# Performance work log

Measured on AMD Instinct MI355X. Metric: run time of the kernel, lower is better.

Reference implementation:

```python
import jax, jax.numpy as jnp
import numpy as np

RADIUS = 0.2
K = 32       # nsample
S = 1024     # npoint
BN_EPS = 1e-5


def fps(xyz, s):
    # xyz: [B, N, 3] -> indices [B, s] (farthest point sampling, start at index 0)
    B, N, _ = xyz.shape

    def step(carry, _):
        dist, last = carry                                  # [B,N], [B]
        lp = jnp.take_along_axis(xyz, last[:, None, None], axis=1)  # [B,1,3]
        d = jnp.sum((xyz - lp) ** 2, axis=-1)               # [B,N]
        dist = jnp.minimum(dist, d)
        nxt = jnp.argmax(dist, axis=-1).astype(jnp.int32)
        return (dist, nxt), last

    init = (jnp.full((B, N), jnp.inf, xyz.dtype), jnp.zeros((B,), jnp.int32))
    _, idxs = jax.lax.scan(step, init, None, length=s)      # [s, B]
    return idxs.T                                           # [B, s]


def query_ball(new_xyz, xyz, radius, k):
    # new_xyz: [B,S,3], xyz: [B,N,3] -> first k in-ball indices [B,S,k]
    B, N, _ = xyz.shape
    d2 = jnp.sum((new_xyz[:, :, None, :] - xyz[:, None, :, :]) ** 2, axis=-1)  # [B,S,N]
    cand = jnp.where(d2 <= radius * radius, jnp.arange(N, dtype=jnp.int32)[None, None, :], N)
    idx = jnp.sort(cand, axis=-1)[..., :k]                  # first-k by index, pytorch3d order
    first = idx[..., :1]
    idx = jnp.where(idx == N, first, idx)                   # replicate first valid index
    return jnp.minimum(idx, N - 1)


def gather_pts(pts, idx):
    # pts: [B,N,C], idx: [B,S,K] -> [B,S,K,C]
    B, N, C = pts.shape
    _, s, k = idx.shape
    g = jnp.take_along_axis(pts, idx.reshape(B, s * k, 1), axis=1)
    return g.reshape(B, s, k, C)


def conv_bn_relu(x, W, b, g, be):
    # x: [B,S,K,Cin], W: [Cout,Cin] (1x1 conv), training-mode BatchNorm over (B,S,K)
    y = jnp.einsum('bskc,oc->bsko', x, W) + b
    mu = jnp.mean(y, axis=(0, 1, 2))
    var = jnp.var(y, axis=(0, 1, 2))
    y = (y - mu) * jax.lax.rsqrt(var + BN_EPS) * g + be
    return jax.nn.relu(y)


def setup_inputs() -> dict:
    key = jax.random.key(0)
    ks = jax.random.split(key, 8)
    B, N, D = 8, 8192, 64
    inp = {
        'xyz': jax.random.uniform(ks[0], (B, 3, N), dtype=jnp.float32),
        'points': jax.random.normal(ks[1], (B, D, N), dtype=jnp.float32),
    }
    dims = [(64, 67), (64, 64), (128, 64)]
    for i, (o, c) in enumerate(dims):
        inp[f'W{i}'] = jax.random.normal(ks[2 + i], (o, c), dtype=jnp.float32) * 0.05
        inp[f'b{i}'] = jnp.zeros((o,), jnp.float32)
        inp[f'g{i}'] = jnp.ones((o,), jnp.float32)
        inp[f'be{i}'] = jnp.zeros((o,), jnp.float32)
    return inp


def reference(xyz, points, W0, b0, g0, be0, W1, b1, g1, be1, W2, b2, g2, be2):
    # xyz: [B,3,N], points: [B,D,N]
    xyz_n = jnp.transpose(xyz, (0, 2, 1))                   # [B,N,3]
    pts_n = jnp.transpose(points, (0, 2, 1))                # [B,N,D]
    idx = fps(xyz_n, S)                                     # [B,S]
    new_xyz = jnp.take_along_axis(xyz_n, idx[..., None], axis=1)  # [B,S,3]
    gidx = query_ball(new_xyz, xyz_n, RADIUS, K)            # [B,S,K]
    gxyz = (gather_pts(xyz_n, gidx) - new_xyz[:, :, None, :]) / RADIUS  # [B,S,K,3]
    gpts = gather_pts(pts_n, gidx)                          # [B,S,K,D]
    feat = jnp.concatenate([gpts, gxyz], axis=-1)           # [B,S,K,D+3]
    feat = conv_bn_relu(feat, W0, b0, g0, be0)
    feat = conv_bn_relu(feat, W1, b1, g1, be1)
    feat = conv_bn_relu(feat, W2, b2, g2, be2)
    new_points = jnp.max(feat, axis=2)                      # [B,S,Cout]
    return (jnp.transpose(new_xyz, (0, 2, 1)), jnp.transpose(new_points, (0, 2, 1)))
```

## Files before the change

### kernel.cpp

```cpp
#include <hip/hip_runtime.h>

#define BB 8
#define NN 8192
#define SS 1024
#define KK 32
#define NPIX (BB*SS*KK)
#define R2C 0.04f
#define EPS 1e-5f

#define FT 1024
#define FW (FT/64)
#define PPT (NN/FT)
#define NCELL 4096
#define TBLK 64

#define OFF_IDX      0u
#define OFF_NEWXYZ   (OFF_IDX + BB*SS*4)
#define OFF_GIDX     (OFF_NEWXYZ + BB*SS*3*4)
#define OFF_XYZN     (OFF_GIDX + BB*SS*KK*4)
#define OFF_PTSN     (OFF_XYZN + BB*NN*3*4)
#define OFF_Y0       (OFF_PTSN + BB*NN*64*4)
#define OFF_Y1       (OFF_Y0 + NPIX*64*2)
#define OFF_MAXMIN   (OFF_Y1 + NPIX*64*2)
#define OFF_P0       (OFF_MAXMIN + BB*SS*128*2*4)
#define OFF_P1       (OFF_P0 + 1024*128*4)
#define OFF_P2       (OFF_P1 + 1024*128*4)
#define OFF_SC       (OFF_P2 + 1024*256*4)

__device__ __forceinline__ unsigned short f2bf(float x){
    unsigned u = __float_as_uint(x);
    unsigned r = (u + 0x7FFFu + ((u >> 16) & 1u)) >> 16;
    return (unsigned short)r;
}
__device__ __forceinline__ float bf2f(unsigned h){
    return __uint_as_float(h << 16);
}
__device__ __forceinline__ float sqdist3(float dx, float dy, float dz){
    return __fadd_rn(__fadd_rn(__fmul_rn(dx,dx), __fmul_rn(dy,dy)), __fmul_rn(dz,dz));
}
__device__ __forceinline__ int spread4(int v){
    return (v&1) | ((v&2)<<2) | ((v&4)<<4) | ((v&8)<<6);
}

template<int CTRL>
__device__ __forceinline__ unsigned long long dpp_max_step(unsigned long long k){
    int lo = (int)(unsigned)k;
    int hi = (int)(unsigned)(k >> 32);
    int olo = __builtin_amdgcn_update_dpp(0, lo, CTRL, 0xf, 0xf, true);
    int ohi = __builtin_amdgcn_update_dpp(0, hi, CTRL, 0xf, 0xf, true);
    unsigned long long o = ((unsigned long long)(unsigned)ohi << 32) | (unsigned)olo;
    return (o > k) ? o : k;
}
__device__ __forceinline__ unsigned long long wave_max_u64(unsigned long long k){
    k = dpp_max_step<0x111>(k);
    k = dpp_max_step<0x112>(k);
    k = dpp_max_step<0x114>(k);
    k = dpp_max_step<0x118>(k);
    k = dpp_max_step<0x142>(k);
    k = dpp_max_step<0x143>(k);
    return k;
}

__global__ __launch_bounds__(FT) void fps_kernel(const float* __restrict__ xyz,
                                                 const float* __restrict__ pts,
                                                 float* __restrict__ newxyz,
                                                 float* __restrict__ out,
                                                 float* __restrict__ xyz_n,
                                                 float* __restrict__ pts_n){
    __shared__ float sx[NN], sy[NN], sz[NN];
    __shared__ int   si[NN];
    __shared__ int   hist[NCELL];
    __shared__ int   waveTot[FW];
    __shared__ unsigned long long cells[SS];
    int tid = threadIdx.x;

    if (blockIdx.x >= 8){
        int gid = (blockIdx.x - 8) * FT + tid;
        int b = gid >> 13, i = gid & (NN - 1);
        const float* xb = xyz + (size_t)b * 3 * NN;
        float x = xb[i], y = xb[NN + i], z = xb[2 * NN + i];
        float* xd = xyz_n + ((size_t)b * NN + i) * 3;
        xd[0] = x; xd[1] = y; xd[2] = z;
        const float* pb = pts + (size_t)b * 64 * NN + i;
        float4* pd = (float4*)(pts_n + ((size_t)b * NN + i) * 64);
#pragma unroll
        for (int q = 0; q < 16; ++q){
            float4 v;
            v.x = pb[(q*4+0)*NN]; v.y = pb[(q*4+1)*NN];
            v.z = pb[(q*4+2)*NN]; v.w = pb[(q*4+3)*NN];
            pd[q] = v;
        }
        return;
    }

    int b = blockIdx.x;
    int wave = tid >> 6, lane = tid & 63;
    const float* xb = xyz + (size_t)b * 3 * NN;

    int cell[PPT];
#pragma unroll
    for (int j = 0; j < PPT; ++j){
        int i = tid + j * FT;
        float x = xb[i], y = xb[NN + i], z = xb[2*NN + i];
        sx[i] = x; sy[i] = y; sz[i] = z;
        int cx = min(15, max(0, (int)(x * 16.f)));
        int cy = min(15, max(0, (int)(y * 16.f)));
        int cz = min(15, max(0, (int)(z * 16.f)));
        cell[j] = spread4(cx) | (spread4(cy) << 1) | (spread4(cz) << 2);
    }
#pragma unroll
    for (int k = 0; k < NCELL/FT; ++k) hist[tid * (NCELL/FT) + k] = 0;
    cells[tid] = 0ull;
    __syncthreads();
#pragma unroll
    for (int j = 0; j < PPT; ++j) atomicAdd(&hist[cell[j]], 1);
    __syncthreads();
    {
        int base0 = tid * (NCELL/FT);
        int sum4 = 0;
#pragma unroll
        for (int k = 0; k < NCELL/FT; ++k) sum4 += hist[base0 + k];
        int s = sum4;
#pragma unroll
        for (int m = 1; m < 64; m <<= 1){
            int v = __shfl_up(s, m);
            if (lane >= m) s += v;
        }
        if (lane == 63) waveTot[wave] = s;
        __syncthreads();
        int wbase = 0;
#pragma unroll
        for (int w2 = 0; w2 < FW; ++w2) if (w2 < wave) wbase += waveTot[w2];
        int run = wbase + s - sum4;
#pragma unroll
        for (int k = 0; k < NCELL/FT; ++k){
            int h = hist[base0 + k];
            hist[base0 + k] = run;
            run += h;
        }
    }
    __syncthreads();
#pragma unroll
    for (int j = 0; j < PPT; ++j){
        int pos = atomicAdd(&hist[cell[j]], 1);
        si[pos] = tid + j * FT;
    }
    __syncthreads();
    float px[PPT], py[PPT], pz[PPT], dist[PPT];
    int oi[PPT];
    float bxmin =  1e30f, bxmax = -1e30f;
    float bymin =  1e30f, bymax = -1e30f;
    float bzmin =  1e30f, bzmax = -1e30f;
#pragma unroll
    for (int j = 0; j < PPT; ++j){
        int g = si[tid * PPT + j];
        oi[j] = g;
        float x = sx[g], y = sy[g], z = sz[g];
        px[j] = x; py[j] = y; pz[j] = z;
        bxmin = fminf(bxmin, x); bxmax = fmaxf(bxmax, x);
        bymin = fminf(bymin, y); bymax = fmaxf(bymax, y);
        bzmin = fminf(bzmin, z); bzmax = fmaxf(bzmax, z);
        dist[j] = __int_as_float(0x7f800000);
    }
    __syncthreads();

    unsigned long long mykey = 0ull;
    unsigned long long lane63cache = 0ull;
    float tmax = __int_as_float(0x7f800000);
    int w = 0;
    for (int t = 0; t < SS; ++t){
        if (tid == 0) hist[t] = w;
        float lx = sx[w], ly = sy[w], lz = sz[w];
        float cdx = __fsub_rn(lx, fminf(fmaxf(lx, bxmin), bxmax));
        float cdy = __fsub_rn(ly, fminf(fmaxf(ly, bymin), bymax));
        float cdz = __fsub_rn(lz, fminf(fmaxf(lz, bzmin), bzmax));
        float d_bb = sqdist3(cdx, cdy, cdz);
        bool active = d_bb < tmax;
        unsigned long long bal = __ballot(active);
        if (active){
            {
#pragma clang fp contract(off)
#pragma unroll
                for (int j = 0; j < PPT; ++j){
                    float dx = px[j] - lx;
                    float dy = py[j] - ly;
                    float dz = pz[j] - lz;
                    float d = ((dx*dx) + (dy*dy)) + (dz*dz);
                    dist[j] = fminf(dist[j], d);
                }
            }
            float m0 = fmaxf(dist[0], dist[1]);
            float m1 = fmaxf(dist[2], dist[3]);
            float m2 = fmaxf(dist[4], dist[5]);
            float m3 = fmaxf(dist[6], dist[7]);
            m0 = fmaxf(m0, m1); m2 = fmaxf(m2, m3);
            float maxd = fmaxf(m0, m2);
            int bo = 0x7fffffff;
#pragma unroll
            for (int j = 0; j < PPT; ++j)
                if (dist[j] == maxd) bo = min(bo, oi[j]);
            mykey = ((unsigned long long)__float_as_uint(maxd) << 32)
                  | (unsigned)(~bo);
            tmax = maxd;
        }
        if (bal){
            unsigned long long k = wave_max_u64(mykey);
            if (lane == 63) lane63cache = k;
        }
        if (lane == 63) atomicMax(&cells[t], lane63cache);
        __syncthreads();
        unsigned long long km = cells[t];
        w = (int)(~(unsigned)km);
    }
    __syncthreads();
    for (int t2 = tid; t2 < SS; t2 += FT){
        int hw = hist[t2];
        float x = sx[hw], y = sy[hw], z = sz[hw];
        out[(size_t)b * 3 * SS + t2]          = x;
        out[(size_t)b * 3 * SS + SS + t2]     = y;
        out[(size_t)b * 3 * SS + 2*SS + t2]   = z;
        float* nw = newxyz + ((size_t)b * SS + t2) * 3;
        nw[0] = x; nw[1] = y; nw[2] = z;
    }
}

__global__ __launch_bounds__(256) void qb_kernel(const float* __restrict__ xyz,
                                                 const float* __restrict__ newxyz,
                                                 int* __restrict__ gidx){
    int wid = (blockIdx.x * 256 + threadIdx.x) >> 6;
    int lane = threadIdx.x & 63;
    int b = wid >> 10;
    const float* nw = newxyz + (size_t)wid * 3;
    float cx = nw[0], cy = nw[1], cz = nw[2];
    const float* xb = xyz + (size_t)b * 3 * NN;
    int total = 0, firstIdx = -1;
    int* gout = gidx + (size_t)wid * KK;
    for (int base = 0; base < NN; base += 64){
        int i = base + lane;
        float dx = __fsub_rn(cx, xb[i]);
        float dy = __fsub_rn(cy, xb[NN + i]);
        float dz = __fsub_rn(cz, xb[2*NN + i]);
        float d2 = sqdist3(dx, dy, dz);
        bool in = (d2 <= R2C);
        unsigned long long m = __ballot(in);
        int pos = total + __popcll(m & ((1ull << lane) - 1ull));
        if (in && pos < KK) gout[pos] = i;
        if (firstIdx < 0 && m) firstIdx = base + (__ffsll((unsigned long long)m) - 1);
        total += __popcll(m);
        if (total >= KK) break;
    }
    if (total < KK){
        int f = (total > 0) ? firstIdx : (NN - 1);
        for (int p = total + lane; p < KK; p += 64) gout[p] = f;
    }
}

__global__ __launch_bounds__(256) void l0_kernel(const float* __restrict__ pts_n,
                                                 const float* __restrict__ xyz_n,
                                                 const float* __restrict__ newxyz,
                                                 const int* __restrict__ gidx,
                                                 const float* __restrict__ W0,
                                                 const float* __restrict__ b0,
                                                 uint4* __restrict__ y0,
                                                 float* __restrict__ part0){
    __shared__ float lsum[4][64][2];
    int tid = threadIdx.x;
    int pixel = blockIdx.x * 256 + tid;
    int sample = pixel >> 5;
    int b = sample >> 10;
    int gi = gidx[pixel];
    int wave = tid >> 6, lane = tid & 63;

    float ff[67];
    const float4* prow = (const float4*)(pts_n + ((size_t)b * NN + gi) * 64);
#pragma unroll
    for (int q = 0; q < 16; ++q){
        float4 v = prow[q];
        ff[q*4] = v.x; ff[q*4+1] = v.y; ff[q*4+2] = v.z; ff[q*4+3] = v.w;
    }
    const float* pr = xyz_n + ((size_t)b * NN + gi) * 3;
    const float* nw = newxyz + (size_t)sample * 3;
    ff[64] = __fsub_rn(pr[0], nw[0]) / 0.2f;
    ff[65] = __fsub_rn(pr[1], nw[1]) / 0.2f;
    ff[66] = __fsub_rn(pr[2], nw[2]) / 0.2f;

    for (int oc = 0; oc < 8; ++oc){
        float acc[8];
#pragma unroll
        for (int j = 0; j < 8; ++j) acc[j] = b0[oc*8+j];
#pragma unroll
        for (int c = 0; c < 67; ++c){
            float fe = ff[c];
#pragma unroll
            for (int j = 0; j < 8; ++j) acc[j] += fe * W0[(oc*8+j)*67 + c];
        }
        uint4 pk;
        unsigned us[8];
#pragma unroll
        for (int j = 0; j < 8; ++j){
            float v = acc[j];
            float s1 = v, s2 = v * v;
#pragma unroll
            for (int m = 1; m <= 32; m <<= 1){
                s1 += __shfl_xor(s1, m);
                s2 += __shfl_xor(s2, m);
            }
            if (lane == 0){ lsum[wave][oc*8+j][0] = s1; lsum[wave][oc*8+j][1] = s2; }
            us[j] = f2bf(v);
        }
        pk.x = us[0] | (us[1] << 16);
        pk.y = us[2] | (us[3] << 16);
        pk.z = us[4] | (us[5] << 16);
        pk.w = us[6] | (us[7] << 16);
        y0[(size_t)pixel * 8 + oc] = pk;
    }
    __syncthreads();
    if (tid < 128){
        float s = lsum[0][tid>>1][tid&1] + lsum[1][tid>>1][tid&1]
                + lsum[2][tid>>1][tid&1] + lsum[3][tid>>1][tid&1];
        part0[(size_t)blockIdx.x * 128 + tid] = s;
    }
}

__global__ __launch_bounds__(256) void l1_kernel(const uint4* __restrict__ y0,
                                                 const float* __restrict__ scale0,
                                                 const float* __restrict__ shift0,
                                                 const float* __restrict__ W1,
                                                 const float* __restrict__ b1,
                                                 uint4* __restrict__ y1,
                                                 float* __restrict__ part1){
    __shared__ float lsum[4][64][2];
    int tid = threadIdx.x;
    int pixel = blockIdx.x * 256 + tid;
    int wave = tid >> 6, lane = tid & 63;

    float x[64];
#pragma unroll
    for (int q = 0; q < 8; ++q){
        uint4 v = y0[(size_t)pixel * 8 + q];
        unsigned w[4] = {v.x, v.y, v.z, v.w};
#pragma unroll
        for (int r = 0; r < 4; ++r){
            int c = q*8 + r*2;
            x[c]   = fmaxf(bf2f(w[r] & 0xFFFFu) * scale0[c]   + shift0[c],   0.f);
            x[c+1] = fmaxf(bf2f(w[r] >> 16)     * scale0[c+1] + shift0[c+1], 0.f);
        }
    }
    for (int oc = 0; oc < 8; ++oc){
        float acc[8];
#pragma unroll
        for (int j = 0; j < 8; ++j) acc[j] = b1[oc*8+j];
#pragma unroll
        for (int c = 0; c < 64; ++c){
            float fe = x[c];
#pragma unroll
            for (int j = 0; j < 8; ++j) acc[j] += fe * W1[(oc*8+j)*64 + c];
        }
        uint4 pk;
        unsigned us[8];
#pragma unroll
        for (int j = 0; j < 8; ++j){
            float v = acc[j];
            float s1 = v, s2 = v * v;
#pragma unroll
            for (int m = 1; m <= 32; m <<= 1){
                s1 += __shfl_xor(s1, m);
                s2 += __shfl_xor(s2, m);
            }
            if (lane == 0){ lsum[wave][oc*8+j][0] = s1; lsum[wave][oc*8+j][1] = s2; }
            us[j] = f2bf(v);
        }
        pk.x = us[0] | (us[1] << 16);
        pk.y = us[2] | (us[3] << 16);
        pk.z = us[4] | (us[5] << 16);
        pk.w = us[6] | (us[7] << 16);
        y1[(size_t)pixel * 8 + oc] = pk;
    }
    __syncthreads();
    if (tid < 128){
        float s = lsum[0][tid>>1][tid&1] + lsum[1][tid>>1][tid&1]
                + lsum[2][tid>>1][tid&1] + lsum[3][tid>>1][tid&1];
        part1[(size_t)blockIdx.x * 128 + tid] = s;
    }
}

__global__ __launch_bounds__(256) void l2_kernel(const uint4* __restrict__ y1,
                                                 const float* __restrict__ scale1,
                                                 const float* __restrict__ shift1,
                                                 const float* __restrict__ W2,
                                                 const float* __restrict__ b2,
                                                 float* __restrict__ maxmin,
                                                 float* __restrict__ part2){
    __shared__ float lsum[4][128][2];
    int tid = threadIdx.x;
    int pixel = blockIdx.x * 256 + tid;
    int sample = pixel >> 5;
    int wave = tid >> 6, lane = tid & 63;

    float x[64];
#pragma unroll
    for (int q = 0; q < 8; ++q){
        uint4 v = y1[(size_t)pixel * 8 + q];
        unsigned w[4] = {v.x, v.y, v.z, v.w};
#pragma unroll
        for (int r = 0; r < 4; ++r){
            int c = q*8 + r*2;
            x[c]   = fmaxf(bf2f(w[r] & 0xFFFFu) * scale1[c]   + shift1[c],   0.f);
            x[c+1] = fmaxf(bf2f(w[r] >> 16)     * scale1[c+1] + shift1[c+1], 0.f);
        }
    }
    for (int oc = 0; oc < 16; ++oc){
        float acc[8];
#pragma unroll
        for (int j = 0; j < 8; ++j) acc[j] = b2[oc*8+j];
#pragma unroll
        for (int c = 0; c < 64; ++c){
            float fe = x[c];
#pragma unroll
            for (int j = 0; j < 8; ++j) acc[j] += fe * W2[(oc*8+j)*64 + c];
        }
#pragma unroll
        for (int j = 0; j < 8; ++j){
            float v = acc[j];
            int ch = oc*8 + j;
            float mx = v, mn = v;
#pragma unroll
            for (int m = 1; m <= 16; m <<= 1){
                mx = fmaxf(mx, __shfl_xor(mx, m));
                mn = fminf(mn, __shfl_xor(mn, m));
            }
            float s1 = v, s2 = v * v;
#pragma unroll
            for (int m = 1; m <= 32; m <<= 1){
                s1 += __shfl_xor(s1, m);
                s2 += __shfl_xor(s2, m);
            }
            if (lane == 0){ lsum[wave][ch][0] = s1; lsum[wave][ch][1] = s2; }
            if ((tid & 31) == 0){
                float* mm = maxmin + ((size_t)sample * 128 + ch) * 2;
                mm[0] = mx; mm[1] = mn;
            }
        }
    }
    __syncthreads();
    {
        float s = lsum[0][tid>>1][tid&1] + lsum[1][tid>>1][tid&1]
                + lsum[2][tid>>1][tid&1] + lsum[3][tid>>1][tid&1];
        part2[(size_t)blockIdx.x * 256 + tid] = s;
    }
}

__global__ __launch_bounds__(1024) void fin_kernel(const float* __restrict__ part, int O,
                           const float* __restrict__ g, const float* __restrict__ be,
                           float* __restrict__ scale, float* __restrict__ shift){
    __shared__ float4 ls[1024];
    int tid = threadIdx.x;
    int M = 2 * O;
    int V = M >> 2;
    int NC = 1024 / V;
    int q = tid & (V - 1);
    int c = tid / V;
    int per = 1024 / NC;
    const float4* p4 = (const float4*)part;
    float4 s = {0.f, 0.f, 0.f, 0.f};
    for (int r = 0; r < per; ++r){
        int blk = c * per + r;
        float4 v = p4[(size_t)blk * V + q];
        s.x += v.x; s.y += v.y; s.z += v.z; s.w += v.w;
    }
    ls[c * V + q] = s;
    __syncthreads();
    if (tid < V){
        float4 t4 = ls[tid];
        for (int c2 = 1; c2 < NC; ++c2){
            float4 v = ls[c2 * V + tid];
            t4.x += v.x; t4.y += v.y; t4.z += v.z; t4.w += v.w;
        }
        float inv = 1.0f / (float)NPIX;
        int ch0 = 2 * tid, ch1 = 2 * tid + 1;
        float mu0 = t4.x * inv;
        float var0 = t4.y * inv - mu0 * mu0;
        float sc0 = (1.0f / sqrtf(var0 + EPS)) * g[ch0];
        scale[ch0] = sc0; shift[ch0] = be[ch0] - mu0 * sc0;
        float mu1 = t4.z * inv;
        float var1 = t4.w * inv - mu1 * mu1;
        float sc1 = (1.0f / sqrtf(var1 + EPS)) * g[ch1];
        scale[ch1] = sc1; shift[ch1] = be[ch1] - mu1 * sc1;
    }
}

__global__ __launch_bounds__(256) void out_kernel(const float* __restrict__ maxmin,
                                                  const float* __restrict__ scale2,
                                                  const float* __restrict__ shift2,
                                                  float* __restrict__ out){
    int gid = blockIdx.x * 256 + threadIdx.x;
    int s = gid & 1023;
    int o = (gid >> 10) & 127;
    int b = gid >> 17;
    int sample = b * 1024 + s;
    float2 mm = ((const float2*)maxmin)[(size_t)sample * 128 + o];
    float sc = scale2[o], sh = shift2[o];
    float v = (sc >= 0.f) ? mm.x : mm.y;
    out[gid] = fmaxf(v * sc + sh, 0.f);
}

extern "C" void kernel_launch(void* const* d_in, const int* in_sizes, int n_in,
                              void* d_out, int out_size, void* d_ws, size_t ws_size,
                              hipStream_t stream) {
    const float* xyz = (const float*)d_in[0];
    const float* pts = (const float*)d_in[1];
    const float* W0 = (const float*)d_in[2];
    const float* b0 = (const float*)d_in[3];
    const float* g0 = (const float*)d_in[4];
    const float* be0 = (const float*)d_in[5];
    const float* W1 = (const float*)d_in[6];
    const float* b1 = (const float*)d_in[7];
    const float* g1 = (const float*)d_in[8];
    const float* be1 = (const float*)d_in[9];
    const float* W2 = (const float*)d_in[10];
    const float* b2 = (const float*)d_in[11];
    const float* g2 = (const float*)d_in[12];
    const float* be2 = (const float*)d_in[13];

    char* ws = (char*)d_ws;
    float* newxyz = (float*)(ws + OFF_NEWXYZ);
    int*   gidx   = (int*)(ws + OFF_GIDX);
    float* xyz_n  = (float*)(ws + OFF_XYZN);
    float* pts_n  = (float*)(ws + OFF_PTSN);
    uint4* y0     = (uint4*)(ws + OFF_Y0);
    uint4* y1     = (uint4*)(ws + OFF_Y1);
    float* maxmin = (float*)(ws + OFF_MAXMIN);
    float* part0  = (float*)(ws + OFF_P0);
    float* part1  = (float*)(ws + OFF_P1);
    float* part2  = (float*)(ws + OFF_P2);
    float* sc     = (float*)(ws + OFF_SC);
    float* scale0 = sc,        *shift0 = sc + 64;
    float* scale1 = sc + 128,  *shift1 = sc + 192;
    float* scale2 = sc + 256,  *shift2 = sc + 384;

    float* out = (float*)d_out;
    float* out_np = out + BB * 3 * SS;

    hipLaunchKernelGGL(fps_kernel, dim3(8 + TBLK), dim3(FT), 0, stream,
                       xyz, pts, newxyz, out, xyz_n, pts_n);
    hipLaunchKernelGGL(qb_kernel, dim3(2048), dim3(256), 0, stream, xyz, newxyz, gidx);
    hipLaunchKernelGGL(l0_kernel, dim3(1024), dim3(256), 0, stream,
                       pts_n, xyz_n, newxyz, gidx, W0, b0, y0, part0);
    hipLaunchKernelGGL(fin_kernel, dim3(1), dim3(1024), 0, stream, part0, 64, g0, be0, scale0, shift0);
    hipLaunchKernelGGL(l1_kernel, dim3(1024), dim3(256), 0, stream,
                       y0, scale0, shift0, W1, b1, y1, part1);
    hipLaunchKernelGGL(fin_kernel, dim3(1), dim3(1024), 0, stream, part1, 64, g1, be1, scale1, shift1);
    hipLaunchKernelGGL(l2_kernel, dim3(1024), dim3(256), 0, stream,
                       y1, scale1, shift1, W2, b2, maxmin, part2);
    hipLaunchKernelGGL(fin_kernel, dim3(1), dim3(1024), 0, stream, part2, 128, g2, be2, scale2, shift2);
    hipLaunchKernelGGL(out_kernel, dim3(4096), dim3(256), 0, stream, maxmin, scale2, shift2, out_np);
}
```

Baseline: 1.241 ms.

## Use DPP wave reductions, packed float2 FPS distance math, interleaved xyz LDS

Replaces shfl_xor butterfly reductions in the conv layers' BN-statistic and max/min reductions with DPP row-shift/broadcast reductions, reading the result from lane 63. In the FPS kernel, stores xyz interleaved in shared memory and packs the per-thread distance update into 2-wide float vectors so the compiler can emit packed FP32 ops. The aim is to cut cross-lane shuffle latency in the conv kernels and halve the ALU instruction count in the serial FPS loop. Risks include DPP ordering changing float summation order and bank conflicts from the stride-3 LDS layout.

```diff
diff --git a/kernel.cpp b/kernel.cpp
--- a/kernel.cpp
+++ b/kernel.cpp
@@ -13,6 +13,8 @@
 #define PPT (NN/FT)
 #define NCELL 4096
 #define TBLK 64
+
+typedef float v2f __attribute__((ext_vector_type(2)));
 
 #define OFF_IDX      0u
 #define OFF_NEWXYZ   (OFF_IDX + BB*SS*4)
@@ -52,13 +54,44 @@
     return (o > k) ? o : k;
 }
 __device__ __forceinline__ unsigned long long wave_max_u64(unsigned long long k){
-    k = dpp_max_step<0x111>(k);
-    k = dpp_max_step<0x112>(k);
-    k = dpp_max_step<0x114>(k);
-    k = dpp_max_step<0x118>(k);
-    k = dpp_max_step<0x142>(k);
-    k = dpp_max_step<0x143>(k);
+    k = dpp_max_step<0x111>(k); k = dpp_max_step<0x112>(k);
+    k = dpp_max_step<0x114>(k); k = dpp_max_step<0x118>(k);
+    k = dpp_max_step<0x142>(k); k = dpp_max_step<0x143>(k);
     return k;
+}
+
+template<int CTRL>
+__device__ __forceinline__ float dpp_sum_step(float v){
+    int o = __builtin_amdgcn_update_dpp(0, __float_as_int(v), CTRL, 0xf, 0xf, true);
+    return v + __int_as_float(o);
+}
+__device__ __forceinline__ float wave_sum_f32(float v){
+    v = dpp_sum_step<0x111>(v); v = dpp_sum_step<0x112>(v);
+    v = dpp_sum_step<0x114>(v); v = dpp_sum_step<0x118>(v);
+    v = dpp_sum_step<0x142>(v); v = dpp_sum_step<0x143>(v);
+    return v;
+}
+template<int CTRL>
+__device__ __forceinline__ float dpp_max_stepf(float v){
+    int o = __builtin_amdgcn_update_dpp(__float_as_int(v), __float_as_int(v), CTRL, 0xf, 0xf, false);
+    return fmaxf(v, __int_as_float(o));
+}
+template<int CTRL>
+__device__ __forceinline__ float dpp_min_stepf(float v){
+    int o = __builtin_amdgcn_update_dpp(__float_as_int(v), __float_as_int(v), CTRL, 0xf, 0xf, false);
+    return fminf(v, __int_as_float(o));
+}
+__device__ __forceinline__ float grp32_max(float v){
+    v = dpp_max_stepf<0x111>(v); v = dpp_max_stepf<0x112>(v);
+    v = dpp_max_stepf<0x114>(v); v = dpp_max_stepf<0x118>(v);
+    v = dpp_max_stepf<0x142>(v);
+    return v;
+}
+__device__ __forceinline__ float grp32_min(float v){
+    v = dpp_min_stepf<0x111>(v); v = dpp_min_stepf<0x112>(v);
+    v = dpp_min_stepf<0x114>(v); v = dpp_min_stepf<0x118>(v);
+    v = dpp_min_stepf<0x142>(v);
+    return v;
 }
 
 __global__ __launch_bounds__(FT) void fps_kernel(const float* __restrict__ xyz,
@@ -67,7 +100,7 @@
                                                  float* __restrict__ out,
                                                  float* __restrict__ xyz_n,
                                                  float* __restrict__ pts_n){
-    __shared__ float sx[NN], sy[NN], sz[NN];
+    __shared__ float sxyz[NN * 3];
     __shared__ int   si[NN];
     __shared__ int   hist[NCELL];
     __shared__ int   waveTot[FW];
@@ -102,7 +135,7 @@
     for (int j = 0; j < PPT; ++j){
         int i = tid + j * FT;
         float x = xb[i], y = xb[NN + i], z = xb[2*NN + i];
-        sx[i] = x; sy[i] = y; sz[i] = z;
+        sxyz[i*3]   = x; sxyz[i*3+1] = y; sxyz[i*3+2] = z;
         int cx = min(15, max(0, (int)(x * 16.f)));
         int cy = min(15, max(0, (int)(y * 16.f)));
         int cz = min(15, max(0, (int)(z * 16.f)));
@@ -146,7 +179,8 @@
         si[pos] = tid + j * FT;
     }
     __syncthreads();
-    float px[PPT], py[PPT], pz[PPT], dist[PPT];
+    v2f px[PPT/2], py[PPT/2], pz[PPT/2];
+    float dist[PPT];
     int oi[PPT];
     float bxmin =  1e30f, bxmax = -1e30f;
     float bymin =  1e30f, bymax = -1e30f;
@@ -155,8 +189,8 @@
     for (int j = 0; j < PPT; ++j){
         int g = si[tid * PPT + j];
         oi[j] = g;
-        float x = sx[g], y = sy[g], z = sz[g];
-        px[j] = x; py[j] = y; pz[j] = z;
+        float x = sxyz[g*3], y = sxyz[g*3+1], z = sxyz[g*3+2];
+        px[j>>1][j&1] = x; py[j>>1][j&1] = y; pz[j>>1][j&1] = z;
         bxmin = fminf(bxmin, x); bxmax = fmaxf(bxmax, x);
         bymin = fminf(bymin, y); bymax = fmaxf(bymax, y);
         bzmin = fminf(bzmin, z); bzmax = fmaxf(bzmax, z);
@@ -170,7 +204,8 @@
     int w = 0;
     for (int t = 0; t < SS; ++t){
         if (tid == 0) hist[t] = w;
-        float lx = sx[w], ly = sy[w], lz = sz[w];
+        int w3 = w * 3;
+        float lx = sxyz[w3], ly = sxyz[w3+1], lz = sxyz[w3+2];
         float cdx = __fsub_rn(lx, fminf(fmaxf(lx, bxmin), bxmax));
         float cdy = __fsub_rn(ly, fminf(fmaxf(ly, bymin), bymax));
         float cdz = __fsub_rn(lz, fminf(fmaxf(lz, bzmin), bzmax));
@@ -180,13 +215,15 @@
         if (active){
             {
 #pragma clang fp contract(off)
-#pragma unroll
-                for (int j = 0; j < PPT; ++j){
-                    float dx = px[j] - lx;
-                    float dy = py[j] - ly;
-                    float dz = pz[j] - lz;
-                    float d = ((dx*dx) + (dy*dy)) + (dz*dz);
-                    dist[j] = fminf(dist[j], d);
+                v2f lx2 = {lx, lx}, ly2 = {ly, ly}, lz2 = {lz, lz};
+#pragma unroll
+                for (int p = 0; p < PPT/2; ++p){
+                    v2f dx = px[p] - lx2;
+                    v2f dy = py[p] - ly2;
+                    v2f dz = pz[p] - lz2;
+                    v2f d  = ((dx*dx) + (dy*dy)) + (dz*dz);
+                    dist[2*p]   = fminf(dist[2*p],   d[0]);
+                    dist[2*p+1] = fminf(dist[2*p+1], d[1]);
                 }
             }
             float m0 = fmaxf(dist[0], dist[1]);
@@ -214,8 +251,8 @@
     }
     __syncthreads();
     for (int t2 = tid; t2 < SS; t2 += FT){
-        int hw = hist[t2];
-        float x = sx[hw], y = sy[hw], z = sz[hw];
+        int hw = hist[t2] * 3;
+        float x = sxyz[hw], y = sxyz[hw+1], z = sxyz[hw+2];
         out[(size_t)b * 3 * SS + t2]          = x;
         out[(size_t)b * 3 * SS + SS + t2]     = y;
         out[(size_t)b * 3 * SS + 2*SS + t2]   = z;
@@ -299,13 +336,9 @@
 #pragma unroll
         for (int j = 0; j < 8; ++j){
             float v = acc[j];
-            float s1 = v, s2 = v * v;
-#pragma unroll
-            for (int m = 1; m <= 32; m <<= 1){
-                s1 += __shfl_xor(s1, m);
-                s2 += __shfl_xor(s2, m);
-            }
-            if (lane == 0){ lsum[wave][oc*8+j][0] = s1; lsum[wave][oc*8+j][1] = s2; }
+            float s1 = wave_sum_f32(v);
+            float s2 = wave_sum_f32(v * v);
+            if (lane == 63){ lsum[wave][oc*8+j][0] = s1; lsum[wave][oc*8+j][1] = s2; }
             us[j] = f2bf(v);
         }
         pk.x = us[0] | (us[1] << 16);
@@ -361,13 +394,9 @@
 #pragma unroll
         for (int j = 0; j < 8; ++j){
             float v = acc[j];
-            float s1 = v, s2 = v * v;
-#pragma unroll
-            for (int m = 1; m <= 32; m <<= 1){
-                s1 += __shfl_xor(s1, m);
-                s2 += __shfl_xor(s2, m);
-            }
-            if (lane == 0){ lsum[wave][oc*8+j][0] = s1; lsum[wave][oc*8+j][1] = s2; }
+            float s1 = wave_sum_f32(v);
+            float s2 = wave_sum_f32(v * v);
+            if (lane == 63){ lsum[wave][oc*8+j][0] = s1; lsum[wave][oc*8+j][1] = s2; }
             us[j] = f2bf(v);
         }
         pk.x = us[0] | (us[1] << 16);
@@ -423,20 +452,12 @@
         for (int j = 0; j < 8; ++j){
             float v = acc[j];
             int ch = oc*8 + j;
-            float mx = v, mn = v;
-#pragma unroll
-            for (int m = 1; m <= 16; m <<= 1){
-                mx = fmaxf(mx, __shfl_xor(mx, m));
-                mn = fminf(mn, __shfl_xor(mn, m));
-            }
-            float s1 = v, s2 = v * v;
-#pragma unroll
-            for (int m = 1; m <= 32; m <<= 1){
-                s1 += __shfl_xor(s1, m);
-                s2 += __shfl_xor(s2, m);
-            }
-            if (lane == 0){ lsum[wave][ch][0] = s1; lsum[wave][ch][1] = s2; }
-            if ((tid & 31) == 0){
+            float mx = grp32_max(v);
+            float mn = grp32_min(v);
+            float s1 = wave_sum_f32(v);
+            float s2 = wave_sum_f32(v * v);
+            if (lane == 63){ lsum[wave][ch][0] = s1; lsum[wave][ch][1] = s2; }
+            if ((tid & 31) == 31){
                 float* mm = maxmin + ((size_t)sample * 128 + ch) * 2;
                 mm[0] = mx; mm[1] = mn;
             }
```

After: 1.238 ms. No clear change (-0.3%).
